# Optimization experiments

Hardware: AMD Instinct MI355X
Metric: run time of the kernel (lower is better)

The kernel has to match this reference:

```python
import jax, jax.numpy as jnp
import numpy as np

B, T, H = 8, 1024, 640
N_PHONE, N_PHONEME = 230, 96


def _make_mapping():
    # 0/1 phone->phoneme allophone map, shape (n_phoneme, n_phone).
    # Every phone maps to >=1 phoneme; every phoneme covered (n_phone > n_phoneme).
    rng = np.random.default_rng(0)
    m = np.zeros((N_PHONEME, N_PHONE), dtype=np.float32)
    cols = np.arange(N_PHONE)
    m[cols % N_PHONEME, cols] = 1.0
    m[rng.integers(0, N_PHONEME, size=N_PHONE), cols] = 1.0  # some phones are allophones of 2 phonemes
    m[0, 0] = 1.0  # blank -> blank, as in allophone_layer
    return jnp.asarray(m)


def setup_inputs() -> dict:
    key = jax.random.key(0)
    k1, k2 = jax.random.split(key)
    enc_output = jax.random.normal(k1, (B, T, H), dtype=jnp.float32)
    feature2phone = jax.random.normal(k2, (H, N_PHONE), dtype=jnp.float32)
    return {"enc_output": enc_output, "feature2phone": feature2phone, "mapping": _make_mapping()}


def reference(enc_output, feature2phone, mapping):
    # phone logits: (B,T,H) @ (H,P) -> (B,T,P), scaled by sqrt(H)
    hidden = feature2phone.shape[0]
    phone = jnp.einsum('bth,hp->btp', enc_output, feature2phone) / jnp.sqrt(jnp.asarray(hidden, enc_output.dtype))
    # broadcast-multiply with 0/1 map -> (B,T,M,P), mask zeros with -inf
    allo = phone[:, :, None, :] * mapping  # mapping: (M,P)
    allo = jnp.where(mapping > 0, allo, -jnp.inf)
    # masked max segment-reduce over the phone axis -> (B,T,M)
    phoneme = jnp.max(allo, axis=-1)
    # log-softmax over phoneme dim
    return jax.nn.log_softmax(phoneme, axis=2)
```

## Files before the change

### kernel.cpp

```cpp
#include <hip/hip_runtime.h>
#include <math.h>

#define NH 640
#define NP 230
#define NM 96
#define NROWS 8192
#define MAXL 32
#define NSTEP 20
#define MBLK 32
#define NBLOCKS (NROWS / MBLK)
#define PFB 8

#define OFF_CNT  0
#define OFF_CSR  4096
#define OFF_B    65536

typedef __bf16 bf16_t;
typedef bf16_t bf16x8 __attribute__((ext_vector_type(8)));
typedef float floatx4 __attribute__((ext_vector_type(4)));

static __device__ __forceinline__ unsigned short f2b(float f) {
    unsigned u = __float_as_uint(f);
    u += 0x7fffu + ((u >> 16) & 1u);
    return (unsigned short)(u >> 16);
}

__global__ __launch_bounds__(256)
void prep_kernel(const float* __restrict__ f2p,
                 const float* __restrict__ mapping,
                 int* __restrict__ cnt, int* __restrict__ csr,
                 unsigned short* __restrict__ wsB2) {
    const int b = blockIdx.x;
    const int tid = threadIdx.x;
    if (b < 24) {
        int wave = b * 4 + (tid >> 6);
        int lane = tid & 63;
        if (wave >= NM) return;
        int base = 0;
        #pragma unroll
        for (int c = 0; c < 4; ++c) {
            int p = c * 64 + lane;
            float v = (p < NP) ? mapping[wave * NP + p] : 0.0f;
            unsigned long long mask = __ballot(v > 0.0f);
            if (v > 0.0f) {
                int idx = base + __popcll(mask & ((1ull << lane) - 1ull));
                if (idx < MAXL) csr[wave * MAXL + idx] = p;
            }
            base += __popcll(mask);
        }
        if (lane == 0) cnt[wave] = base < MAXL ? base : MAXL;
    } else {
        int g = (b - 24) * 256 + tid;
        int m16  = g & 15;
        int quad = (g >> 4) & 3;
        int ct   = (g >> 6) & 15;
        int s    = g >> 10;
        int n = ct * 16 + m16;
        int k0 = s * 32 + quad * 8;
        unsigned short v[8];
        #pragma unroll
        for (int j = 0; j < 8; ++j)
            v[j] = (n < NP) ? f2b(f2p[(size_t)(k0 + j) * NP + n]) : (unsigned short)0;
        *(uint4*)(wsB2 + (size_t)g * 8) = *(const uint4*)v;
    }
}

__global__ __launch_bounds__(512, 2)
void fused_phonetics_kernel(const float* __restrict__ enc,
                            const unsigned short* __restrict__ wsB2,
                            const int* __restrict__ cnt,
                            const int* __restrict__ csr,
                            float* __restrict__ out) {
    __shared__ __align__(16) unsigned short sA[2560 * 8];
    __shared__ int scnt[NM];
    __shared__ int scsr[NM * MAXL];
    float (*phone)[257] = (float (*)[257])sA;

    const int tid  = threadIdx.x;
    const int lane = tid & 63;
    const int wv   = tid >> 6;
    const int m16  = lane & 15;
    const int quad = lane >> 4;
    const int row0 = blockIdx.x * MBLK;

    float4 areg[10];
    #pragma unroll
    for (int i = 0; i < 10; ++i)
        areg[i] = *(const float4*)(enc + (size_t)row0 * NH + i * 2048 + tid * 4);

    const unsigned short* bptr = wsB2 + ((size_t)(wv * 2) * 64 + lane) * 8;
    uint4 bpre[2 * PFB];
    #pragma unroll
    for (int s = 0; s < PFB; ++s) {
        bpre[2 * s + 0] = *(const uint4*)(bptr + ((size_t)s * 16 + 0) * 64 * 8);
        bpre[2 * s + 1] = *(const uint4*)(bptr + ((size_t)s * 16 + 1) * 64 * 8);
    }

    if (tid < NM) scnt[tid] = cnt[tid];
    #pragma unroll
    for (int j = 0; j < 6; ++j)
        scsr[tid + j * 512] = csr[tid + j * 512];

    #pragma unroll
    for (int i = 0; i < 10; ++i) {
        int F = i * 2048 + tid * 4;
        int row = F / 640;
        int k   = F - row * 640;
        int s  = k >> 5;
        int q  = (k & 31) >> 3;
        int j0 = k & 7;
        unsigned short v[4];
        v[0] = f2b(areg[i].x); v[1] = f2b(areg[i].y);
        v[2] = f2b(areg[i].z); v[3] = f2b(areg[i].w);
        int soff = ((s * 2 + (row >> 4)) * 64 + q * 16 + (row & 15)) * 8 + j0;
        *(uint2*)(sA + soff) = *(const uint2*)v;
    }
    __syncthreads();

    floatx4 acc00 = {0.f,0.f,0.f,0.f}, acc01 = acc00, acc10 = acc00, acc11 = acc00;

    const unsigned short* aptr = sA + (size_t)lane * 8;

    #pragma unroll
    for (int s = 0; s < NSTEP; ++s) {
        uint4 a0 = *(const uint4*)(aptr + (size_t)(s * 2 + 0) * 64 * 8);
        uint4 a1 = *(const uint4*)(aptr + (size_t)(s * 2 + 1) * 64 * 8);
        uint4 b0, b1;
        if (s < PFB) {
            b0 = bpre[2 * s + 0];
            b1 = bpre[2 * s + 1];
        } else {
            b0 = *(const uint4*)(bptr + ((size_t)s * 16 + 0) * 64 * 8);
            b1 = *(const uint4*)(bptr + ((size_t)s * 16 + 1) * 64 * 8);
        }
        bf16x8 A0 = __builtin_bit_cast(bf16x8, a0);
        bf16x8 A1 = __builtin_bit_cast(bf16x8, a1);
        bf16x8 B0 = __builtin_bit_cast(bf16x8, b0);
        bf16x8 B1 = __builtin_bit_cast(bf16x8, b1);
        acc00 = __builtin_amdgcn_mfma_f32_16x16x32_bf16(A0, B0, acc00, 0, 0, 0);
        acc01 = __builtin_amdgcn_mfma_f32_16x16x32_bf16(A0, B1, acc01, 0, 0, 0);
        acc10 = __builtin_amdgcn_mfma_f32_16x16x32_bf16(A1, B0, acc10, 0, 0, 0);
        acc11 = __builtin_amdgcn_mfma_f32_16x16x32_bf16(A1, B1, acc11, 0, 0, 0);
    }

    __syncthreads();

    const float scale = 0.03952847075210474f;
    #pragma unroll
    for (int i = 0; i < 4; ++i) {
        int r = quad * 4 + i;
        phone[r     ][wv * 32 +  0 + m16] = acc00[i] * scale;
        phone[r     ][wv * 32 + 16 + m16] = acc01[i] * scale;
        phone[r + 16][wv * 32 +  0 + m16] = acc10[i] * scale;
        phone[r + 16][wv * 32 + 16 + m16] = acc11[i] * scale;
    }
    __syncthreads();

    const int r   = tid >> 4;
    const int l16 = tid & 15;
    float pmv[6];
    float mx = -INFINITY;
    #pragma unroll
    for (int j = 0; j < 6; ++j) {
        int m = l16 + j * 16;
        int c = scnt[m];
        const int* lst = scsr + m * MAXL;
        float best = -INFINITY;
        for (int jj = 0; jj < c; ++jj) best = fmaxf(best, phone[r][lst[jj]]);
        pmv[j] = best;
        mx = fmaxf(mx, best);
    }
    #pragma unroll
    for (int d = 1; d < 16; d <<= 1) mx = fmaxf(mx, __shfl_xor(mx, d));
    float s = 0.f;
    #pragma unroll
    for (int j = 0; j < 6; ++j) s += __expf(pmv[j] - mx);
    #pragma unroll
    for (int d = 1; d < 16; d <<= 1) s += __shfl_xor(s, d);
    const float lse = mx + __logf(s);
    #pragma unroll
    for (int j = 0; j < 6; ++j)
        out[(size_t)(row0 + r) * NM + l16 + j * 16] = pmv[j] - lse;
}

extern "C" void kernel_launch(void* const* d_in, const int* in_sizes, int n_in,
                              void* d_out, int out_size, void* d_ws, size_t ws_size,
                              hipStream_t stream) {
    const float* enc     = (const float*)d_in[0];
    const float* f2p     = (const float*)d_in[1];
    const float* mapping = (const float*)d_in[2];
    float* out = (float*)d_out;

    char* ws = (char*)d_ws;
    int* cnt = (int*)(ws + OFF_CNT);
    int* csr = (int*)(ws + OFF_CSR);
    unsigned short* wsB2 = (unsigned short*)(ws + OFF_B);

    prep_kernel<<<104, 256, 0, stream>>>(f2p, mapping, cnt, csr, wsB2);
    fused_phonetics_kernel<<<NBLOCKS, 512, 0, stream>>>(enc, wsB2, cnt, csr, out);
}
```

Measured before the change: 82.30 us.

## Merge prep and main kernels into one cooperative launch with grid sync

Folds the weight bf16 repacking and mapping-to-CSR construction into the main kernel. Each block does a slice of the prep work while its activation tile is loading, then a grid-wide barrier makes the shared workspace visible before the MFMA loop. This removes a second kernel launch and the gap between the two kernels. In exchange it requires all 256 blocks to be co-resident and pays for a grid sync. It also delays the B-fragment prefetch until after the barrier.

```diff
diff --git a/kernel.cpp b/kernel.cpp
--- a/kernel.cpp
+++ b/kernel.cpp
@@ -1,4 +1,5 @@
 #include <hip/hip_runtime.h>
+#include <hip/hip_cooperative_groups.h>
 #include <math.h>
 
 #define NH 640
@@ -10,6 +11,7 @@
 #define MBLK 32
 #define NBLOCKS (NROWS / MBLK)
 #define PFB 8
+#define FRAGS_PER_BLK 80
 
 #define OFF_CNT  0
 #define OFF_CSR  4096
@@ -18,6 +20,8 @@
 typedef __bf16 bf16_t;
 typedef bf16_t bf16x8 __attribute__((ext_vector_type(8)));
 typedef float floatx4 __attribute__((ext_vector_type(4)));
+
+namespace cg = cooperative_groups;
 
 static __device__ __forceinline__ unsigned short f2b(float f) {
     unsigned u = __float_as_uint(f);
@@ -25,52 +29,14 @@
     return (unsigned short)(u >> 16);
 }
 
-__global__ __launch_bounds__(256)
-void prep_kernel(const float* __restrict__ f2p,
-                 const float* __restrict__ mapping,
-                 int* __restrict__ cnt, int* __restrict__ csr,
-                 unsigned short* __restrict__ wsB2) {
-    const int b = blockIdx.x;
-    const int tid = threadIdx.x;
-    if (b < 24) {
-        int wave = b * 4 + (tid >> 6);
-        int lane = tid & 63;
-        if (wave >= NM) return;
-        int base = 0;
-        #pragma unroll
-        for (int c = 0; c < 4; ++c) {
-            int p = c * 64 + lane;
-            float v = (p < NP) ? mapping[wave * NP + p] : 0.0f;
-            unsigned long long mask = __ballot(v > 0.0f);
-            if (v > 0.0f) {
-                int idx = base + __popcll(mask & ((1ull << lane) - 1ull));
-                if (idx < MAXL) csr[wave * MAXL + idx] = p;
-            }
-            base += __popcll(mask);
-        }
-        if (lane == 0) cnt[wave] = base < MAXL ? base : MAXL;
-    } else {
-        int g = (b - 24) * 256 + tid;
-        int m16  = g & 15;
-        int quad = (g >> 4) & 3;
-        int ct   = (g >> 6) & 15;
-        int s    = g >> 10;
-        int n = ct * 16 + m16;
-        int k0 = s * 32 + quad * 8;
-        unsigned short v[8];
-        #pragma unroll
-        for (int j = 0; j < 8; ++j)
-            v[j] = (n < NP) ? f2b(f2p[(size_t)(k0 + j) * NP + n]) : (unsigned short)0;
-        *(uint4*)(wsB2 + (size_t)g * 8) = *(const uint4*)v;
-    }
-}
-
 __global__ __launch_bounds__(512, 2)
-void fused_phonetics_kernel(const float* __restrict__ enc,
-                            const unsigned short* __restrict__ wsB2,
-                            const int* __restrict__ cnt,
-                            const int* __restrict__ csr,
-                            float* __restrict__ out) {
+void fused_all_kernel(const float* __restrict__ enc,
+                      const float* __restrict__ f2p,
+                      const float* __restrict__ mapping,
+                      unsigned short* __restrict__ wsB2,
+                      int* __restrict__ cnt,
+                      int* __restrict__ csr,
+                      float* __restrict__ out) {
     __shared__ __align__(16) unsigned short sA[2560 * 8];
     __shared__ int scnt[NM];
     __shared__ int scsr[NM * MAXL];
@@ -81,25 +47,60 @@
     const int wv   = tid >> 6;
     const int m16  = lane & 15;
     const int quad = lane >> 4;
-    const int row0 = blockIdx.x * MBLK;
+    const int b    = blockIdx.x;
+    const int row0 = b * MBLK;
+
+    const bool doB = (tid < FRAGS_PER_BLK);
+    const int  pg  = b * FRAGS_PER_BLK + tid;
+    float pf[8];
+    int pn = 0;
+    if (doB) {
+        int m16p = pg & 15;
+        int qd   = (pg >> 4) & 3;
+        int ct   = (pg >> 6) & 15;
+        int sp   = pg >> 10;
+        pn = ct * 16 + m16p;
+        int k0 = sp * 32 + qd * 8;
+        #pragma unroll
+        for (int j = 0; j < 8; ++j)
+            pf[j] = (pn < NP) ? f2p[(size_t)(k0 + j) * NP + pn] : 0.0f;
+    }
+
+    const bool doC = (b < NM) && (tid < 64);
+    float mv[4];
+    if (doC) {
+        #pragma unroll
+        for (int c = 0; c < 4; ++c) {
+            int p = c * 64 + lane;
+            mv[c] = (p < NP) ? mapping[b * NP + p] : 0.0f;
+        }
+    }
 
     float4 areg[10];
     #pragma unroll
     for (int i = 0; i < 10; ++i)
         areg[i] = *(const float4*)(enc + (size_t)row0 * NH + i * 2048 + tid * 4);
 
-    const unsigned short* bptr = wsB2 + ((size_t)(wv * 2) * 64 + lane) * 8;
-    uint4 bpre[2 * PFB];
-    #pragma unroll
-    for (int s = 0; s < PFB; ++s) {
-        bpre[2 * s + 0] = *(const uint4*)(bptr + ((size_t)s * 16 + 0) * 64 * 8);
-        bpre[2 * s + 1] = *(const uint4*)(bptr + ((size_t)s * 16 + 1) * 64 * 8);
-    }
-
-    if (tid < NM) scnt[tid] = cnt[tid];
-    #pragma unroll
-    for (int j = 0; j < 6; ++j)
-        scsr[tid + j * 512] = csr[tid + j * 512];
+    if (doB) {
+        unsigned short v[8];
+        #pragma unroll
+        for (int j = 0; j < 8; ++j) v[j] = f2b(pf[j]);
+        *(uint4*)(wsB2 + (size_t)pg * 8) = *(const uint4*)v;
+    }
+
+    if (doC) {
+        int base = 0;
+        #pragma unroll
+        for (int c = 0; c < 4; ++c) {
+            unsigned long long mask = __ballot(mv[c] > 0.0f);
+            if (mv[c] > 0.0f) {
+                int idx = base + __popcll(mask & ((1ull << lane) - 1ull));
+                if (idx < MAXL) csr[b * MAXL + idx] = c * 64 + lane;
+            }
+            base += __popcll(mask);
+        }
+        if (lane == 0) cnt[b] = base < MAXL ? base : MAXL;
+    }
 
     #pragma unroll
     for (int i = 0; i < 10; ++i) {
@@ -115,10 +116,23 @@
         int soff = ((s * 2 + (row >> 4)) * 64 + q * 16 + (row & 15)) * 8 + j0;
         *(uint2*)(sA + soff) = *(const uint2*)v;
     }
-    __syncthreads();
+
+    cg::this_grid().sync();
+
+    int creg[6];
+    #pragma unroll
+    for (int j = 0; j < 6; ++j) creg[j] = csr[tid + j * 512];
+    int cc = (tid < NM) ? cnt[tid] : 0;
+
+    const unsigned short* bptr = wsB2 + ((size_t)(wv * 2) * 64 + lane) * 8;
+    uint4 bpre[2 * PFB];
+    #pragma unroll
+    for (int s = 0; s < PFB; ++s) {
+        bpre[2 * s + 0] = *(const uint4*)(bptr + ((size_t)s * 16 + 0) * 64 * 8);
+        bpre[2 * s + 1] = *(const uint4*)(bptr + ((size_t)s * 16 + 1) * 64 * 8);
+    }
 
     floatx4 acc00 = {0.f,0.f,0.f,0.f}, acc01 = acc00, acc10 = acc00, acc11 = acc00;
-
     const unsigned short* aptr = sA + (size_t)lane * 8;
 
     #pragma unroll
@@ -154,6 +168,9 @@
         phone[r + 16][wv * 32 +  0 + m16] = acc10[i] * scale;
         phone[r + 16][wv * 32 + 16 + m16] = acc11[i] * scale;
     }
+    #pragma unroll
+    for (int j = 0; j < 6; ++j) scsr[tid + j * 512] = creg[j];
+    if (tid < NM) scnt[tid] = cc;
     __syncthreads();
 
     const int r   = tid >> 4;
@@ -196,6 +213,7 @@
     int* csr = (int*)(ws + OFF_CSR);
     unsigned short* wsB2 = (unsigned short*)(ws + OFF_B);
 
-    prep_kernel<<<104, 256, 0, stream>>>(f2p, mapping, cnt, csr, wsB2);
-    fused_phonetics_kernel<<<NBLOCKS, 512, 0, stream>>>(enc, wsB2, cnt, csr, out);
+    void* args[] = {&enc, &f2p, &mapping, &wsB2, &cnt, &csr, &out};
+    hipLaunchCooperativeKernel((const void*)fused_all_kernel,
+                               dim3(NBLOCKS), dim3(512), args, 0, stream);
 }
```

After: 120.6 us. 1.46x slower.

## Split activation staging into two K halves overlapping conversion with MFMA

Applied to the files above, without the earlier changes.

The fused kernel now loads the encoder tile as two K halves. It converts and stores the first half to shared memory, runs the first ten MFMA steps, then converts the second half and runs the remaining steps. All B fragments are held in registers, with more prefetched up front, and the CSR loads are hoisted ahead of the activation loads. The aim is to overlap the bf16 conversion and LDS stores with matrix math, and to hide global B-load latency, at the cost of much higher register pressure and possible lower occupancy.

```diff
diff --git a/kernel.cpp b/kernel.cpp
--- a/kernel.cpp
+++ b/kernel.cpp
@@ -9,7 +9,7 @@
 #define NSTEP 20
 #define MBLK 32
 #define NBLOCKS (NROWS / MBLK)
-#define PFB 8
+#define PFB 14
 
 #define OFF_CNT  0
 #define OFF_CSR  4096
@@ -83,60 +83,104 @@
     const int quad = lane >> 4;
     const int row0 = blockIdx.x * MBLK;
 
-    float4 areg[10];
-    #pragma unroll
-    for (int i = 0; i < 10; ++i)
-        areg[i] = *(const float4*)(enc + (size_t)row0 * NH + i * 2048 + tid * 4);
+    int creg[6];
+    #pragma unroll
+    for (int j = 0; j < 6; ++j) creg[j] = csr[tid + j * 512];
+    int cc = (tid < NM) ? cnt[tid] : 0;
+
+    float4 areg0[5], areg1[5];
+    #pragma unroll
+    for (int i = 0; i < 5; ++i) {
+        int G = i * 8192 + tid * 16;
+        int row = G / 1280;
+        int cb4 = (G - row * 1280) >> 2;
+        areg0[i] = *(const float4*)(enc + (size_t)(row0 + row) * NH + cb4);
+    }
+    #pragma unroll
+    for (int i = 0; i < 5; ++i) {
+        int G = i * 8192 + tid * 16;
+        int row = G / 1280;
+        int cb4 = (G - row * 1280) >> 2;
+        areg1[i] = *(const float4*)(enc + (size_t)(row0 + row) * NH + 320 + cb4);
+    }
 
     const unsigned short* bptr = wsB2 + ((size_t)(wv * 2) * 64 + lane) * 8;
-    uint4 bpre[2 * PFB];
+    uint4 bpre[2 * NSTEP];
     #pragma unroll
     for (int s = 0; s < PFB; ++s) {
         bpre[2 * s + 0] = *(const uint4*)(bptr + ((size_t)s * 16 + 0) * 64 * 8);
         bpre[2 * s + 1] = *(const uint4*)(bptr + ((size_t)s * 16 + 1) * 64 * 8);
     }
 
-    if (tid < NM) scnt[tid] = cnt[tid];
-    #pragma unroll
-    for (int j = 0; j < 6; ++j)
-        scsr[tid + j * 512] = csr[tid + j * 512];
-
-    #pragma unroll
-    for (int i = 0; i < 10; ++i) {
-        int F = i * 2048 + tid * 4;
-        int row = F / 640;
-        int k   = F - row * 640;
+    #pragma unroll
+    for (int j = 0; j < 6; ++j) scsr[tid + j * 512] = creg[j];
+    if (tid < NM) scnt[tid] = cc;
+
+    #pragma unroll
+    for (int i = 0; i < 5; ++i) {
+        int G = i * 8192 + tid * 16;
+        int row = G / 1280;
+        int cb4 = (G - row * 1280) >> 2;
+        int k = cb4;
         int s  = k >> 5;
         int q  = (k & 31) >> 3;
         int j0 = k & 7;
         unsigned short v[4];
-        v[0] = f2b(areg[i].x); v[1] = f2b(areg[i].y);
-        v[2] = f2b(areg[i].z); v[3] = f2b(areg[i].w);
+        v[0] = f2b(areg0[i].x); v[1] = f2b(areg0[i].y);
+        v[2] = f2b(areg0[i].z); v[3] = f2b(areg0[i].w);
         int soff = ((s * 2 + (row >> 4)) * 64 + q * 16 + (row & 15)) * 8 + j0;
         *(uint2*)(sA + soff) = *(const uint2*)v;
     }
     __syncthreads();
 
+    #pragma unroll
+    for (int s = PFB; s < NSTEP; ++s) {
+        bpre[2 * s + 0] = *(const uint4*)(bptr + ((size_t)s * 16 + 0) * 64 * 8);
+        bpre[2 * s + 1] = *(const uint4*)(bptr + ((size_t)s * 16 + 1) * 64 * 8);
+    }
+
     floatx4 acc00 = {0.f,0.f,0.f,0.f}, acc01 = acc00, acc10 = acc00, acc11 = acc00;
-
     const unsigned short* aptr = sA + (size_t)lane * 8;
 
     #pragma unroll
-    for (int s = 0; s < NSTEP; ++s) {
+    for (int s = 0; s < 10; ++s) {
         uint4 a0 = *(const uint4*)(aptr + (size_t)(s * 2 + 0) * 64 * 8);
         uint4 a1 = *(const uint4*)(aptr + (size_t)(s * 2 + 1) * 64 * 8);
-        uint4 b0, b1;
-        if (s < PFB) {
-            b0 = bpre[2 * s + 0];
-            b1 = bpre[2 * s + 1];
-        } else {
-            b0 = *(const uint4*)(bptr + ((size_t)s * 16 + 0) * 64 * 8);
-            b1 = *(const uint4*)(bptr + ((size_t)s * 16 + 1) * 64 * 8);
-        }
         bf16x8 A0 = __builtin_bit_cast(bf16x8, a0);
         bf16x8 A1 = __builtin_bit_cast(bf16x8, a1);
-        bf16x8 B0 = __builtin_bit_cast(bf16x8, b0);
-        bf16x8 B1 = __builtin_bit_cast(bf16x8, b1);
+        bf16x8 B0 = __builtin_bit_cast(bf16x8, bpre[2 * s + 0]);
+        bf16x8 B1 = __builtin_bit_cast(bf16x8, bpre[2 * s + 1]);
+        acc00 = __builtin_amdgcn_mfma_f32_16x16x32_bf16(A0, B0, acc00, 0, 0, 0);
+        acc01 = __builtin_amdgcn_mfma_f32_16x16x32_bf16(A0, B1, acc01, 0, 0, 0);
+        acc10 = __builtin_amdgcn_mfma_f32_16x16x32_bf16(A1, B0, acc10, 0, 0, 0);
+        acc11 = __builtin_amdgcn_mfma_f32_16x16x32_bf16(A1, B1, acc11, 0, 0, 0);
+    }
+
+    #pragma unroll
+    for (int i = 0; i < 5; ++i) {
+        int G = i * 8192 + tid * 16;
+        int row = G / 1280;
+        int cb4 = (G - row * 1280) >> 2;
+        int k = 320 + cb4;
+        int s  = k >> 5;
+        int q  = (k & 31) >> 3;
+        int j0 = k & 7;
+        unsigned short v[4];
+        v[0] = f2b(areg1[i].x); v[1] = f2b(areg1[i].y);
+        v[2] = f2b(areg1[i].z); v[3] = f2b(areg1[i].w);
+        int soff = ((s * 2 + (row >> 4)) * 64 + q * 16 + (row & 15)) * 8 + j0;
+        *(uint2*)(sA + soff) = *(const uint2*)v;
+    }
+    __syncthreads();
+
+    #pragma unroll
+    for (int s = 10; s < NSTEP; ++s) {
+        uint4 a0 = *(const uint4*)(aptr + (size_t)(s * 2 + 0) * 64 * 8);
+        uint4 a1 = *(const uint4*)(aptr + (size_t)(s * 2 + 1) * 64 * 8);
+        bf16x8 A0 = __builtin_bit_cast(bf16x8, a0);
+        bf16x8 A1 = __builtin_bit_cast(bf16x8, a1);
+        bf16x8 B0 = __builtin_bit_cast(bf16x8, bpre[2 * s + 0]);
+        bf16x8 B1 = __builtin_bit_cast(bf16x8, bpre[2 * s + 1]);
         acc00 = __builtin_amdgcn_mfma_f32_16x16x32_bf16(A0, B0, acc00, 0, 0, 0);
         acc01 = __builtin_amdgcn_mfma_f32_16x16x32_bf16(A0, B1, acc01, 0, 0, 0);
         acc10 = __builtin_amdgcn_mfma_f32_16x16x32_bf16(A1, B0, acc10, 0, 0, 0);
```

Result: no change. 80.82 us (-1.8%).
